# Kernel tuning notes

Measured on AMD Instinct MI355X. Metric: run time of the kernel, lower is better.

The kernel has to match this reference:

```python
import jax, jax.numpy as jnp
import numpy as np

B, S, D, H = 4, 4096, 1024, 64

def setup_inputs() -> dict:
    key = jax.random.key(0)
    k1, k2, k3, k4 = jax.random.split(key, 4)
    x = jax.random.normal(k1, (B, S, D), dtype=jnp.float32)
    scale = D ** -0.5
    Wq = jax.random.normal(k2, (D, H), dtype=jnp.float32) * scale
    Wk = jax.random.normal(k3, (D, H), dtype=jnp.float32) * scale
    Wv = jax.random.normal(k4, (D, H), dtype=jnp.float32) * scale
    return {"x": x, "Wq": Wq, "Wk": Wk, "Wv": Wv}

def reference(x, Wq, Wk, Wv):
    # Projections: [B,S,D] @ [D,H] -> [B,S,H]
    Q = jnp.einsum('bsd,dh->bsh', x, Wq)
    K = jnp.einsum('bsd,dh->bsh', x, Wk)
    V = jnp.einsum('bsd,dh->bsh', x, Wv)
    H_ = Q.shape[-1]
    # Scores [B,S,S], scaled by head_size**-0.5
    scores = jnp.einsum('bqh,bkh->bqk', Q, K) * (H_ ** -0.5)
    attn = jax.nn.softmax(scores, axis=-1)
    return jnp.einsum('bqk,bkh->bqh', attn, V)
```

## Files before the change

kernel.cpp:

```cpp
#include <hip/hip_runtime.h>
#include <hip/hip_bf16.h>

#define B_ 4
#define S_ 4096
#define D_ 1024
#define H_ 64

typedef __attribute__((ext_vector_type(8))) short bf16x8;
typedef __attribute__((ext_vector_type(4))) float f32x4;

static __device__ __forceinline__ unsigned short f2bf(float f) {
    union { float f; unsigned int i; } v; v.f = f;
    unsigned int r = v.i + 0x7FFFu + ((v.i >> 16) & 1u);
    return (unsigned short)(r >> 16);
}

typedef __attribute__((address_space(3))) unsigned int lds_u32;
typedef __attribute__((address_space(1))) const unsigned int glb_u32;
static __device__ __forceinline__ void gload16(const void* g, void* l) {
    __builtin_amdgcn_global_load_lds((glb_u32*)g, (lds_u32*)l, 16, 0, 0);
}

__global__ __launch_bounds__(256) void prep_w(
    const float* __restrict__ Wq, const float* __restrict__ Wk,
    const float* __restrict__ Wv, unsigned short* __restrict__ WF)
{
    __shared__ float wt[256][64];
    const int bid = blockIdx.x;
    const int y = bid >> 2, kr = (bid & 3) * 256;
    const float* W = (y == 0) ? Wq : (y == 1) ? Wk : Wv;
    const float scale = (y == 0) ? 0.125f * 1.4426950408889634f : 1.0f;
    const int t = threadIdx.x;

    #pragma unroll
    for (int it = 0; it < 16; ++it) {
        int idx = it * 256 + t;
        int k = idx >> 4, h4 = (idx & 15) * 4;
        *(float4*)&wt[k][h4] = *(const float4*)(W + (size_t)(kr + k) * H_ + h4);
    }
    __syncthreads();

    const int ntl = t >> 6, l = t & 63, lm = l & 15, lg = l >> 4;
    const int h = ntl * 16 + lm;
    #pragma unroll
    for (int g = 0; g < 8; ++g) {
        bf16x8 v;
        #pragma unroll
        for (int e = 0; e < 8; ++e) v[e] = f2bf(wt[g * 32 + lg * 8 + e][h] * scale);
        int ntg = y * 4 + ntl, gg = (kr >> 5) + g;
        *(bf16x8*)(WF + ((size_t)(ntg * 32 + gg) * 64 + l) * 8) = v;
    }
}

__global__ __launch_bounds__(512) void proj_mfma(
    const float* __restrict__ x, const unsigned short* __restrict__ WF,
    unsigned short* __restrict__ Qw, unsigned short* __restrict__ Kw,
    unsigned short* __restrict__ Vtw)
{
    __shared__ __align__(16) char pool[65536];

    const int tid = threadIdx.x;
    const int w = tid >> 6, l = tid & 63;
    const int lm = l & 15, lg = l >> 4;
    const int wm = w >> 2, wn = w & 3;
    const int row0 = blockIdx.x * 64;

    f32x4 acc[2][3];
    #pragma unroll
    for (int mt = 0; mt < 2; ++mt)
        #pragma unroll
        for (int n = 0; n < 3; ++n) acc[mt][n] = (f32x4){0.f, 0.f, 0.f, 0.f};

    auto stage = [&](int t) {
        #pragma unroll
        for (int j = 0; j < 2; ++j) {
            int i = (w * 2 + j) * 64 + l;
            int row = i >> 4;
            int u = ((i & 15) << 4) ^ ((row & 7) << 4);
            const char* g = (const char*)x + ((size_t)(row0 + row) << 12) + (t << 8) + u;
            char* dst = pool + (t & 3) * 16384 + ((w * 2 + j) << 10);
            gload16(g, dst);
        }
    };

    auto loadB = [&](int t, bf16x8* bf) {
        #pragma unroll
        for (int n = 0; n < 3; ++n)
            #pragma unroll
            for (int gg = 0; gg < 2; ++gg)
                bf[n * 2 + gg] = *(const bf16x8*)(WF +
                    ((size_t)((wn * 3 + n) * 32 + (t * 2 + gg)) * 64 + l) * 8);
    };

    auto compute = [&](int t, const bf16x8* bf) {
        const char* base = pool + (t & 3) * 16384;
        #pragma unroll
        for (int gg = 0; gg < 2; ++gg) {
            bf16x8 af[2];
            #pragma unroll
            for (int mt = 0; mt < 2; ++mt) {
                int r = wm * 32 + mt * 16 + lm;
                int sw = (r & 7) << 4;
                int c0 = gg * 128 + lg * 32;
                f32x4 a0 = *(const f32x4*)(base + r * 256 + (c0 ^ sw));
                f32x4 a1 = *(const f32x4*)(base + r * 256 + ((c0 + 16) ^ sw));
                af[mt][0] = f2bf(a0[0]); af[mt][1] = f2bf(a0[1]);
                af[mt][2] = f2bf(a0[2]); af[mt][3] = f2bf(a0[3]);
                af[mt][4] = f2bf(a1[0]); af[mt][5] = f2bf(a1[1]);
                af[mt][6] = f2bf(a1[2]); af[mt][7] = f2bf(a1[3]);
            }
            #pragma unroll
            for (int mt = 0; mt < 2; ++mt)
                #pragma unroll
                for (int n = 0; n < 3; ++n)
                    acc[mt][n] = __builtin_amdgcn_mfma_f32_16x16x32_bf16(
                        af[mt], bf[n * 2 + gg], acc[mt][n], 0, 0, 0);
        }
    };

    bf16x8 bA[6], bB[6];
    stage(0); stage(1); loadB(0, bA);

    #pragma unroll
    for (int tt = 0; tt < 16; tt += 2) {
        if (tt + 2 < 16) stage(tt + 2);
        loadB(tt + 1, bB);
        if (tt < 14) { asm volatile("s_waitcnt vmcnt(8)" ::: "memory"); }
        else         { asm volatile("s_waitcnt vmcnt(6)" ::: "memory"); }
        __builtin_amdgcn_sched_barrier(0);
        __builtin_amdgcn_s_barrier();
        __builtin_amdgcn_sched_barrier(0);
        compute(tt, bA);

        if (tt + 3 < 16) stage(tt + 3);
        if (tt + 2 < 16) loadB(tt + 2, bA);
        if (tt + 2 < 16) { asm volatile("s_waitcnt vmcnt(8)" ::: "memory"); }
        else             { asm volatile("s_waitcnt vmcnt(0)" ::: "memory"); }
        __builtin_amdgcn_sched_barrier(0);
        __builtin_amdgcn_s_barrier();
        __builtin_amdgcn_sched_barrier(0);
        compute(tt + 1, bB);
    }

    __syncthreads();
    unsigned short* et = (unsigned short*)pool;
    #pragma unroll
    for (int mt = 0; mt < 2; ++mt)
        #pragma unroll
        for (int n = 0; n < 3; ++n)
            #pragma unroll
            for (int reg = 0; reg < 4; ++reg)
                et[(wm * 32 + mt * 16 + lg * 4 + reg) * 200 + (wn * 48 + n * 16 + lm)] =
                    f2bf(acc[mt][n][reg]);
    __syncthreads();

    #pragma unroll
    for (int p = 0; p < 2; ++p) {
        int r = tid >> 3;
        int c = ((tid & 7) + p * 8) * 8;
        bf16x8 v = *(const bf16x8*)(et + r * 200 + c);
        unsigned short* dst = (c < 64) ? Qw : Kw;
        *(bf16x8*)(dst + (size_t)(row0 + r) * H_ + (c & 63)) = v;
    }
    {
        int h = tid & 63, i0 = (tid >> 6) * 8;
        bf16x8 v;
        #pragma unroll
        for (int i = 0; i < 8; ++i) v[i] = et[(i0 + i) * 200 + 128 + h];
        int bat = row0 >> 12, s0 = (row0 & (S_ - 1)) + i0;
        *(bf16x8*)(Vtw + ((size_t)bat * H_ + h) * S_ + s0) = v;
    }
}

__global__ __launch_bounds__(256) void attn_kernel(
    const unsigned short* __restrict__ Qg, const unsigned short* __restrict__ Kg,
    const unsigned short* __restrict__ Vtg,
    float* __restrict__ Op, float2* __restrict__ Ml, int chunk)
{
    __shared__ __align__(16) char kv_lds[2][16384];
    __shared__ __align__(16) unsigned short pt[4][1024];

    const int tid = threadIdx.x;
    const int l = tid & 63, w = tid >> 6;
    const int lm = l & 15, lg = l >> 4;
    const int b = blockIdx.y, z = blockIdx.z;
    const int q0 = blockIdx.x * 64;
    const int kvbase = z * chunk;
    const int ntile = chunk >> 6;

    bf16x8 qa[2];
    {
        const unsigned short* qp = Qg + ((size_t)(b * S_ + q0 + w * 16 + lm)) * H_ + lg * 8;
        qa[0] = *(const bf16x8*)qp;
        qa[1] = *(const bf16x8*)(qp + 32);
    }

    f32x4 oa[4];
    #pragma unroll
    for (int nt = 0; nt < 4; ++nt) oa[nt] = (f32x4){0.f, 0.f, 0.f, 0.f};
    float m = -INFINITY, lsum = 0.f;
    unsigned short* ptw = pt[w];

    const char* Kb = (const char*)Kg + ((size_t)b * S_ + kvbase) * (H_ * 2);
    const char* Vb = (const char*)Vtg + ((size_t)b * H_) * (S_ * 2) + (size_t)kvbase * 2;

    auto stage = [&](int t, int buf) {
        #pragma unroll
        for (int j = 0; j < 2; ++j) {
            int slot = w * 2 + j;
            int row = slot * 8 + (l >> 3), c16 = l & 7;
            int u = (c16 * 16) ^ ((row & 7) << 4);
            gload16(Kb + (size_t)(t * 64 + row) * 128 + u,
                    &kv_lds[buf][slot * 1024]);
            gload16(Vb + (size_t)row * (S_ * 2) + t * 128 + u,
                    &kv_lds[buf][8192 + slot * 1024]);
        }
    };

    stage(0, 0);
    asm volatile("s_waitcnt vmcnt(0)" ::: "memory");
    __builtin_amdgcn_s_barrier();

    for (int t = 0; t < ntile; ++t) {
        const int cur = t & 1;
        if (t + 1 < ntile) stage(t + 1, cur ^ 1);

        const char* kbase = kv_lds[cur];
        const char* vbase = kv_lds[cur] + 8192;

        f32x4 sv[4];
        #pragma unroll
        for (int nt = 0; nt < 4; ++nt) {
            f32x4 a = (f32x4){0.f, 0.f, 0.f, 0.f};
            int r = nt * 16 + lm, sw = (r & 7) << 4;
            #pragma unroll
            for (int g2 = 0; g2 < 2; ++g2) {
                bf16x8 kb = *(const bf16x8*)(kbase + r * 128 + ((g2 * 64 + lg * 16) ^ sw));
                a = __builtin_amdgcn_mfma_f32_16x16x32_bf16(kb, qa[g2], a, 0, 0, 0);
            }
            sv[nt] = a;
        }

        float tmax = sv[0][0];
        #pragma unroll
        for (int nt = 0; nt < 4; ++nt)
            #pragma unroll
            for (int reg = 0; reg < 4; ++reg) tmax = fmaxf(tmax, sv[nt][reg]);
        tmax = fmaxf(tmax, __shfl_xor(tmax, 16));
        tmax = fmaxf(tmax, __shfl_xor(tmax, 32));
        float mn = fmaxf(m, tmax);
        float sc = exp2f(m - mn);
        m = mn;
        float p[4][4];
        float rs = 0.f;
        #pragma unroll
        for (int nt = 0; nt < 4; ++nt)
            #pragma unroll
            for (int reg = 0; reg < 4; ++reg) {
                p[nt][reg] = exp2f(sv[nt][reg] - mn);
                rs += p[nt][reg];
            }
        rs += __shfl_xor(rs, 16);
        rs += __shfl_xor(rs, 32);
        lsum = lsum * sc + rs;
        #pragma unroll
        for (int nt = 0; nt < 4; ++nt) {
            oa[nt][0] *= sc; oa[nt][1] *= sc; oa[nt][2] *= sc; oa[nt][3] *= sc;
        }

        #pragma unroll
        for (int nt = 0; nt < 4; ++nt)
            #pragma unroll
            for (int j = 0; j < 2; ++j) {
                unsigned int w32;
                asm("v_cvt_pk_bf16_f32 %0, %1, %2"
                    : "=v"(w32) : "v"(p[nt][2 * j]), "v"(p[nt][2 * j + 1]));
                *(unsigned int*)((char*)ptw + lm * 128 +
                                 ((nt * 32 + lg * 8 + j * 4) ^ ((lm & 7) << 4))) = w32;
            }
        asm volatile("s_waitcnt lgkmcnt(0)" ::: "memory");
        __builtin_amdgcn_sched_barrier(0);

        #pragma unroll
        for (int kk = 0; kk < 2; ++kk) {
            bf16x8 pb = *(const bf16x8*)((const char*)ptw + lm * 128 +
                                         ((kk * 64 + lg * 16) ^ ((lm & 7) << 4)));
            #pragma unroll
            for (int nt = 0; nt < 4; ++nt) {
                int hr = nt * 16 + lm;
                bf16x8 vb = *(const bf16x8*)(vbase + hr * 128 +
                                             ((kk * 64 + lg * 16) ^ ((hr & 7) << 4)));
                oa[nt] = __builtin_amdgcn_mfma_f32_16x16x32_bf16(vb, pb, oa[nt], 0, 0, 0);
            }
        }

        asm volatile("s_waitcnt vmcnt(0)" ::: "memory");
        __builtin_amdgcn_sched_barrier(0);
        __builtin_amdgcn_s_barrier();
        __builtin_amdgcn_sched_barrier(0);
    }

    const size_t zb = (size_t)z * B_ + b;
    const size_t qrow = zb * S_ + q0 + w * 16 + lm;
    #pragma unroll
    for (int nt = 0; nt < 4; ++nt)
        *(f32x4*)(Op + qrow * H_ + nt * 16 + lg * 4) = oa[nt];
    if (lg == 0) Ml[qrow] = make_float2(m, lsum);
}

__global__ __launch_bounds__(256) void combine_kernel(
    const float* __restrict__ Op, const float2* __restrict__ Ml,
    float* __restrict__ out, int nsplit)
{
    const int idx = blockIdx.x * 256 + threadIdx.x;
    const int bq = idx >> 4;
    const int h4 = (idx & 15) * 4;
    const size_t BS = (size_t)B_ * S_;

    float M = -INFINITY;
    for (int i = 0; i < nsplit; ++i) M = fmaxf(M, Ml[i * BS + bq].x);
    float L = 0.f;
    float4 acc = make_float4(0.f, 0.f, 0.f, 0.f);
    for (int i = 0; i < nsplit; ++i) {
        float2 ml = Ml[i * BS + bq];
        float wgt = exp2f(ml.x - M);
        L += wgt * ml.y;
        float4 o = *(const float4*)(Op + (i * BS + bq) * H_ + h4);
        acc.x += wgt * o.x; acc.y += wgt * o.y; acc.z += wgt * o.z; acc.w += wgt * o.w;
    }
    float inv = 1.f / L;
    float4 r = make_float4(acc.x * inv, acc.y * inv, acc.z * inv, acc.w * inv);
    *(float4*)(out + (size_t)bq * H_ + h4) = r;
}

extern "C" void kernel_launch(void* const* d_in, const int* in_sizes, int n_in,
                              void* d_out, int out_size, void* d_ws, size_t ws_size,
                              hipStream_t stream) {
    const float* x  = (const float*)d_in[0];
    const float* Wq = (const float*)d_in[1];
    const float* Wk = (const float*)d_in[2];
    const float* Wv = (const float*)d_in[3];

    const size_t NQ = (size_t)B_ * S_ * H_;
    unsigned short* Qw  = (unsigned short*)d_ws;
    unsigned short* Kw  = Qw + NQ;
    unsigned short* Vtw = Kw + NQ;
    unsigned short* WFw = Vtw + NQ;
    char* p = (char*)(WFw + 192 * D_);

    const size_t per_split = NQ * 4 + (size_t)B_ * S_ * 8;
    size_t used = 3 * NQ * 2 + 192 * D_ * 2;
    int nsplit = 4;
    while (nsplit > 1 && used + (size_t)nsplit * per_split > ws_size) nsplit >>= 1;

    float*  Op = (float*)p;
    float2* Ml = (float2*)(p + (size_t)nsplit * NQ * 4);
    float* out = (float*)d_out;

    prep_w<<<12, 256, 0, stream>>>(Wq, Wk, Wv, WFw);

    proj_mfma<<<B_ * S_ / 64, 512, 0, stream>>>(x, WFw, Qw, Kw, Vtw);

    dim3 agrid(S_ / 64, B_, nsplit);
    attn_kernel<<<agrid, 256, 0, stream>>>(Qw, Kw, Vtw, Op, Ml, S_ / nsplit);

    dim3 cgrid(B_ * S_ * 16 / 256);
    combine_kernel<<<cgrid, 256, 0, stream>>>(Op, Ml, out, nsplit);
}
```

Before: 74.86 us.

## Process two query sub-tiles per wave and skip rescale when max barely grows

Each wave now handles 32 query rows instead of 16, so the K and V fragments read from LDS are reused by two MFMA chains and the block covers 128 queries, halving the attention grid. It also adds lazy softmax rescaling: the running max and the accumulator rescale are only updated when the tile max exceeds the stored max by more than 8 (log2 units), which cuts exp and multiply work. This costs more registers and halves the number of blocks (64 per batch/split), which may lower occupancy and CU fill. Skipped rescales leave probabilities up to 2^8 in bf16/fp32; this is mathematically exact after normalisation but risks overflow headroom.

```diff
diff --git a/kernel.cpp b/kernel.cpp
--- a/kernel.cpp
+++ b/kernel.cpp
@@ -178,27 +178,33 @@
     float* __restrict__ Op, float2* __restrict__ Ml, int chunk)
 {
     __shared__ __align__(16) char kv_lds[2][16384];
-    __shared__ __align__(16) unsigned short pt[4][1024];
+    __shared__ __align__(16) unsigned short pt[4][2048];
 
     const int tid = threadIdx.x;
     const int l = tid & 63, w = tid >> 6;
     const int lm = l & 15, lg = l >> 4;
     const int b = blockIdx.y, z = blockIdx.z;
-    const int q0 = blockIdx.x * 64;
+    const int q0 = blockIdx.x * 128;
     const int kvbase = z * chunk;
     const int ntile = chunk >> 6;
 
-    bf16x8 qa[2];
-    {
-        const unsigned short* qp = Qg + ((size_t)(b * S_ + q0 + w * 16 + lm)) * H_ + lg * 8;
-        qa[0] = *(const bf16x8*)qp;
-        qa[1] = *(const bf16x8*)(qp + 32);
-    }
-
-    f32x4 oa[4];
-    #pragma unroll
-    for (int nt = 0; nt < 4; ++nt) oa[nt] = (f32x4){0.f, 0.f, 0.f, 0.f};
-    float m = -INFINITY, lsum = 0.f;
+    bf16x8 qa[2][2];
+    #pragma unroll
+    for (int qb = 0; qb < 2; ++qb) {
+        const unsigned short* qp =
+            Qg + ((size_t)(b * S_ + q0 + w * 32 + qb * 16 + lm)) * H_ + lg * 8;
+        qa[qb][0] = *(const bf16x8*)qp;
+        qa[qb][1] = *(const bf16x8*)(qp + 32);
+    }
+
+    f32x4 oa[2][4];
+    float m[2], lsum[2];
+    #pragma unroll
+    for (int qb = 0; qb < 2; ++qb) {
+        #pragma unroll
+        for (int nt = 0; nt < 4; ++nt) oa[qb][nt] = (f32x4){0.f, 0.f, 0.f, 0.f};
+        m[qb] = -INFINITY; lsum[qb] = 0.f;
+    }
     unsigned short* ptw = pt[w];
 
     const char* Kb = (const char*)Kg + ((size_t)b * S_ + kvbase) * (H_ * 2);
@@ -228,69 +234,83 @@
         const char* kbase = kv_lds[cur];
         const char* vbase = kv_lds[cur] + 8192;
 
-        f32x4 sv[4];
+        f32x4 sv[2][4];
         #pragma unroll
         for (int nt = 0; nt < 4; ++nt) {
-            f32x4 a = (f32x4){0.f, 0.f, 0.f, 0.f};
             int r = nt * 16 + lm, sw = (r & 7) << 4;
-            #pragma unroll
-            for (int g2 = 0; g2 < 2; ++g2) {
-                bf16x8 kb = *(const bf16x8*)(kbase + r * 128 + ((g2 * 64 + lg * 16) ^ sw));
-                a = __builtin_amdgcn_mfma_f32_16x16x32_bf16(kb, qa[g2], a, 0, 0, 0);
+            bf16x8 kb0 = *(const bf16x8*)(kbase + r * 128 + ((lg * 16) ^ sw));
+            bf16x8 kb1 = *(const bf16x8*)(kbase + r * 128 + ((64 + lg * 16) ^ sw));
+            #pragma unroll
+            for (int qb = 0; qb < 2; ++qb) {
+                f32x4 a = (f32x4){0.f, 0.f, 0.f, 0.f};
+                a = __builtin_amdgcn_mfma_f32_16x16x32_bf16(kb0, qa[qb][0], a, 0, 0, 0);
+                a = __builtin_amdgcn_mfma_f32_16x16x32_bf16(kb1, qa[qb][1], a, 0, 0, 0);
+                sv[qb][nt] = a;
             }
-            sv[nt] = a;
-        }
-
-        float tmax = sv[0][0];
-        #pragma unroll
-        for (int nt = 0; nt < 4; ++nt)
-            #pragma unroll
-            for (int reg = 0; reg < 4; ++reg) tmax = fmaxf(tmax, sv[nt][reg]);
-        tmax = fmaxf(tmax, __shfl_xor(tmax, 16));
-        tmax = fmaxf(tmax, __shfl_xor(tmax, 32));
-        float mn = fmaxf(m, tmax);
-        float sc = exp2f(m - mn);
-        m = mn;
-        float p[4][4];
-        float rs = 0.f;
-        #pragma unroll
-        for (int nt = 0; nt < 4; ++nt)
-            #pragma unroll
-            for (int reg = 0; reg < 4; ++reg) {
-                p[nt][reg] = exp2f(sv[nt][reg] - mn);
-                rs += p[nt][reg];
+        }
+
+        #pragma unroll
+        for (int qb = 0; qb < 2; ++qb) {
+            float tmax = sv[qb][0][0];
+            #pragma unroll
+            for (int nt = 0; nt < 4; ++nt)
+                #pragma unroll
+                for (int reg = 0; reg < 4; ++reg) tmax = fmaxf(tmax, sv[qb][nt][reg]);
+            tmax = fmaxf(tmax, __shfl_xor(tmax, 16));
+            tmax = fmaxf(tmax, __shfl_xor(tmax, 32));
+            if (!__all(tmax - m[qb] <= 8.f)) {
+                float mn = fmaxf(m[qb], tmax);
+                float sc = exp2f(m[qb] - mn);
+                m[qb] = mn;
+                lsum[qb] *= sc;
+                #pragma unroll
+                for (int nt = 0; nt < 4; ++nt) {
+                    oa[qb][nt][0] *= sc; oa[qb][nt][1] *= sc;
+                    oa[qb][nt][2] *= sc; oa[qb][nt][3] *= sc;
+                }
             }
-        rs += __shfl_xor(rs, 16);
-        rs += __shfl_xor(rs, 32);
-        lsum = lsum * sc + rs;
-        #pragma unroll
-        for (int nt = 0; nt < 4; ++nt) {
-            oa[nt][0] *= sc; oa[nt][1] *= sc; oa[nt][2] *= sc; oa[nt][3] *= sc;
-        }
-
-        #pragma unroll
-        for (int nt = 0; nt < 4; ++nt)
-            #pragma unroll
-            for (int j = 0; j < 2; ++j) {
-                unsigned int w32;
-                asm("v_cvt_pk_bf16_f32 %0, %1, %2"
-                    : "=v"(w32) : "v"(p[nt][2 * j]), "v"(p[nt][2 * j + 1]));
-                *(unsigned int*)((char*)ptw + lm * 128 +
-                                 ((nt * 32 + lg * 8 + j * 4) ^ ((lm & 7) << 4))) = w32;
-            }
+            float p[4][4];
+            float rs = 0.f;
+            #pragma unroll
+            for (int nt = 0; nt < 4; ++nt)
+                #pragma unroll
+                for (int reg = 0; reg < 4; ++reg) {
+                    p[nt][reg] = exp2f(sv[qb][nt][reg] - m[qb]);
+                    rs += p[nt][reg];
+                }
+            rs += __shfl_xor(rs, 16);
+            rs += __shfl_xor(rs, 32);
+            lsum[qb] += rs;
+            #pragma unroll
+            for (int nt = 0; nt < 4; ++nt)
+                #pragma unroll
+                for (int j = 0; j < 2; ++j) {
+                    unsigned int w32;
+                    asm("v_cvt_pk_bf16_f32 %0, %1, %2"
+                        : "=v"(w32) : "v"(p[nt][2 * j]), "v"(p[nt][2 * j + 1]));
+                    *(unsigned int*)((char*)ptw + (qb * 16 + lm) * 128 +
+                                     ((nt * 32 + lg * 8 + j * 4) ^ ((lm & 7) << 4))) = w32;
+                }
+        }
         asm volatile("s_waitcnt lgkmcnt(0)" ::: "memory");
         __builtin_amdgcn_sched_barrier(0);
 
         #pragma unroll
         for (int kk = 0; kk < 2; ++kk) {
-            bf16x8 pb = *(const bf16x8*)((const char*)ptw + lm * 128 +
-                                         ((kk * 64 + lg * 16) ^ ((lm & 7) << 4)));
+            bf16x8 pb[2];
+            #pragma unroll
+            for (int qb = 0; qb < 2; ++qb)
+                pb[qb] = *(const bf16x8*)((const char*)ptw + (qb * 16 + lm) * 128 +
+                                          ((kk * 64 + lg * 16) ^ ((lm & 7) << 4)));
             #pragma unroll
             for (int nt = 0; nt < 4; ++nt) {
                 int hr = nt * 16 + lm;
                 bf16x8 vb = *(const bf16x8*)(vbase + hr * 128 +
                                              ((kk * 64 + lg * 16) ^ ((hr & 7) << 4)));
-                oa[nt] = __builtin_amdgcn_mfma_f32_16x16x32_bf16(vb, pb, oa[nt], 0, 0, 0);
+                #pragma unroll
+                for (int qb = 0; qb < 2; ++qb)
+                    oa[qb][nt] = __builtin_amdgcn_mfma_f32_16x16x32_bf16(
+                        vb, pb[qb], oa[qb][nt], 0, 0, 0);
             }
         }
 
@@ -301,11 +321,14 @@
     }
 
     const size_t zb = (size_t)z * B_ + b;
-    const size_t qrow = zb * S_ + q0 + w * 16 + lm;
-    #pragma unroll
-    for (int nt = 0; nt < 4; ++nt)
-        *(f32x4*)(Op + qrow * H_ + nt * 16 + lg * 4) = oa[nt];
-    if (lg == 0) Ml[qrow] = make_float2(m, lsum);
+    #pragma unroll
+    for (int qb = 0; qb < 2; ++qb) {
+        const size_t qrow = zb * S_ + q0 + w * 32 + qb * 16 + lm;
+        #pragma unroll
+        for (int nt = 0; nt < 4; ++nt)
+            *(f32x4*)(Op + qrow * H_ + nt * 16 + lg * 4) = oa[qb][nt];
+        if (lg == 0) Ml[qrow] = make_float2(m[qb], lsum[qb]);
+    }
 }
 
 __global__ __launch_bounds__(256) void combine_kernel(
@@ -361,7 +384,7 @@
 
     proj_mfma<<<B_ * S_ / 64, 512, 0, stream>>>(x, WFw, Qw, Kw, Vtw);
 
-    dim3 agrid(S_ / 64, B_, nsplit);
+    dim3 agrid(S_ / 128, B_, nsplit);
     attn_kernel<<<agrid, 256, 0, stream>>>(Qw, Kw, Vtw, Op, Ml, S_ / nsplit);
 
     dim3 cgrid(B_ * S_ * 16 / 256);
```

Result: no change. 75.76 us (+1.2%).
